# Kernel tuning notes

Hardware: AMD Instinct MI355X
Metric: run time of the kernel (lower is better)

The kernel has to match this reference:

```python
import jax, jax.numpy as jnp
import numpy as np

N_NODES = 50000


def gcn_conv(x, W, b, src, dst, n_nodes):
    # PyG GCNConv: h = D^{-1/2}(A+I)D^{-1/2} X W + b, with self-loops added.
    h = x @ W                                   # [N, H]
    loops = jnp.arange(n_nodes, dtype=src.dtype)
    s = jnp.concatenate([src, loops])           # [E+N]
    d = jnp.concatenate([dst, loops])
    deg = jax.ops.segment_sum(jnp.ones_like(d, dtype=h.dtype), d, num_segments=n_nodes)
    dinv = jnp.where(deg > 0, jax.lax.rsqrt(deg), 0.0)
    norm = dinv[s] * dinv[d]                    # [E+N]
    msg = h[s] * norm[:, None]                  # gather + scale
    agg = jax.ops.segment_sum(msg, d, num_segments=n_nodes)  # scatter-add
    return agg + b


def setup_inputs() -> dict:
    key = jax.random.key(0)
    ks = jax.random.split(key, 8)
    N, E, D, H, ED = N_NODES, 800000, 64, 64, 16
    sc = lambda f_in: 1.0 / np.sqrt(f_in)
    return {
        "x": jax.random.normal(ks[0], (N, D), dtype=jnp.float32),
        "src": jax.random.randint(ks[1], (E,), 0, N),
        "dst": jax.random.randint(ks[2], (E,), 0, N),
        "edge_attr": jax.random.normal(ks[3], (E, ED), dtype=jnp.float32),
        "W1": jax.random.normal(ks[4], (D, H), dtype=jnp.float32) * sc(D),
        "b1": jnp.zeros((H,), dtype=jnp.float32),
        "Wm1": jax.random.normal(ks[5], (2 * H + ED, H), dtype=jnp.float32) * sc(2 * H + ED),
        "bm1": jnp.zeros((H,), dtype=jnp.float32),
        "Wm2": jax.random.normal(ks[6], (H, 1), dtype=jnp.float32) * sc(H),
        "bm2": jnp.zeros((1,), dtype=jnp.float32),
    }


def reference(x, src, dst, edge_attr, W1, b1, Wm1, bm1, Wm2, bm2):
    h = jax.nn.relu(gcn_conv(x, W1, b1, src, dst, N_NODES))  # [N, H]
    edge_repr = jnp.concatenate([h[src], h[dst], edge_attr], axis=1)  # [E, 2H+ED]
    hidden = jax.nn.relu(edge_repr @ Wm1 + bm1)
    scores = jax.nn.sigmoid(hidden @ Wm2 + bm2)
    return scores.squeeze(-1)
```

## Files before the change

kernel.cpp:

```cpp
#include <hip/hip_runtime.h>
#include <math.h>


typedef __attribute__((ext_vector_type(8))) short bf16x8;
typedef __attribute__((ext_vector_type(4))) float f32x4;

#define MAXDEG 64
#define BSHIFT 7
#define BMASK 127
#define NBUCK 391
#define CAP 2560
#define CHUNK 2048
#define BINB 391
#define GEMB 782
#define BPB 40

__device__ __forceinline__ unsigned short f2b(float f) {
    unsigned u = __float_as_uint(f);
    unsigned r = (u + 0x7FFFu + ((u >> 16) & 1u)) >> 16;
    return (unsigned short)r;
}

__global__ void __launch_bounds__(256) bin_gemm_pack(
        const int* __restrict__ dst, const int* __restrict__ src,
        unsigned int* __restrict__ region, int* __restrict__ gcur, int E,
        const float* __restrict__ x, const float* __restrict__ W1,
        unsigned short* __restrict__ gbf,
        const float* __restrict__ Wm1, unsigned short* __restrict__ Bp, int N) {
    __shared__ __align__(16) char smem[8192];
    const int bid = blockIdx.x, tid = threadIdx.x;

    if (bid < BINB) {
        int* lc = (int*)smem;
        int* gb = lc + NBUCK;
        for (int i = tid; i < NBUCK; i += 256) lc[i] = 0;
        __syncthreads();
        int base = bid * CHUNK + tid * 8;
        unsigned key[8], val[8];
#pragma unroll
        for (int k = 0; k < 8; ++k) {
            int e = base + k;
            key[k] = 0xFFFFFFFFu;
            if (e < E) {
                int d = dst[e], s = src[e];
                int b = d >> BSHIFT;
                int r = atomicAdd(&lc[b], 1);
                key[k] = (unsigned)b | ((unsigned)r << 9);
                val[k] = ((unsigned)(d & BMASK) << 16) | (unsigned)s;
            }
        }
        __syncthreads();
        for (int i = tid; i < NBUCK; i += 256) {
            int t = lc[i];
            gb[i] = t ? atomicAdd(&gcur[i], t) : 0;
        }
        __syncthreads();
#pragma unroll
        for (int k = 0; k < 8; ++k) {
            if (key[k] != 0xFFFFFFFFu) {
                int b = (int)(key[k] & 511u), r = (int)(key[k] >> 9);
                int idx = gb[b] + r;
                if (idx < CAP) region[(size_t)b * CAP + idx] = val[k];
            }
        }
    } else if (bid < BINB + GEMB) {
        unsigned short* sB = (unsigned short*)smem;
        for (int i = tid; i < 4096; i += 256) {
            int j = i & 7, ln = (i >> 3) & 63, t = (i >> 9) & 3, s = i >> 11;
            int k = s * 32 + (ln >> 4) * 8 + j, col = t * 16 + (ln & 15);
            sB[i] = f2b(W1[k * 64 + col]);
        }
        __syncthreads();
        int wid = (bid - BINB) * 4 + (tid >> 6);
        int NWT = N / 16;
        if (wid < NWT) {
            int lane = tid & 63, m = lane & 15, quad = lane >> 4;
            int r0 = wid * 16;
            f32x4 acc[4];
#pragma unroll
            for (int t = 0; t < 4; ++t) acc[t] = (f32x4){0.f, 0.f, 0.f, 0.f};
            const bf16x8* bp = (const bf16x8*)sB;
#pragma unroll
            for (int s = 0; s < 2; ++s) {
                const float4* xp = (const float4*)(x + (size_t)(r0 + m) * 64 + s * 32 + quad * 8);
                float4 v0 = xp[0], v1 = xp[1];
                bf16x8 a;
                a[0] = (short)f2b(v0.x); a[1] = (short)f2b(v0.y);
                a[2] = (short)f2b(v0.z); a[3] = (short)f2b(v0.w);
                a[4] = (short)f2b(v1.x); a[5] = (short)f2b(v1.y);
                a[6] = (short)f2b(v1.z); a[7] = (short)f2b(v1.w);
#pragma unroll
                for (int t = 0; t < 4; ++t)
                    acc[t] = __builtin_amdgcn_mfma_f32_16x16x32_bf16(
                        a, bp[(s * 4 + t) * 64 + lane], acc[t], 0, 0, 0);
            }
#pragma unroll
            for (int reg = 0; reg < 4; ++reg) {
                int row = r0 + quad * 4 + reg;
#pragma unroll
                for (int t = 0; t < 4; ++t)
                    gbf[(size_t)row * 64 + t * 16 + m] = f2b(acc[t][reg]);
            }
        }
    } else {
        int idx = (bid - BINB - GEMB) * 256 + tid;
        if (idx < 10240) {
            int j = idx & 7, ln = (idx >> 3) & 63, t = (idx >> 9) & 3, s = idx >> 11;
            int k = s * 32 + (ln >> 4) * 8 + j, col = t * 16 + (ln & 15);
            float v = (k < 144) ? Wm1[k * 64 + col] : 0.0f;
            Bp[idx] = f2b(v);
        }
    }
}

__global__ void __launch_bounds__(256) build_csr(
        const unsigned int* __restrict__ region, const int* __restrict__ gcur,
        int* __restrict__ cnt, unsigned short* __restrict__ csr_pad, int N) {
    __shared__ unsigned short lcsr[128 * MAXDEG];
    __shared__ int lcnt[128];
    int b = blockIdx.x, tid = threadIdx.x;
    if (tid < 128) lcnt[tid] = 0;
    __syncthreads();
    int ecnt = gcur[b]; if (ecnt > CAP) ecnt = CAP;
    const unsigned int* reg = region + (size_t)b * CAP;
    for (int i = tid; i < ecnt; i += 256) {
        unsigned v = reg[i];
        int dloc = (int)(v >> 16), s = (int)(v & 0xFFFFu);
        int r = atomicAdd(&lcnt[dloc], 1);
        if (r < MAXDEG) lcsr[dloc * MAXDEG + r] = (unsigned short)s;
    }
    __syncthreads();
    int n0 = b << BSHIFT;
    int nb = N - n0; if (nb > 128) nb = 128;
    if (tid < nb) cnt[n0 + tid] = lcnt[tid];
    int4* gout = (int4*)(csr_pad + (size_t)n0 * MAXDEG);
    const int4* lin = (const int4*)lcsr;
    int tot = nb * 8;
    for (int i = tid; i < tot; i += 256) gout[i] = lin[i];
}

__global__ void __launch_bounds__(256) gather_finalize(
        const unsigned short* __restrict__ gbf, const unsigned short* __restrict__ csr_pad,
        const int* __restrict__ cnt, const float* __restrict__ b1,
        unsigned short* __restrict__ hbf, int N) {
    int wid = blockIdx.x * 4 + (threadIdx.x >> 6);
    if (wid >= N) return;
    int lane = threadIdx.x & 63;
    int n8 = lane >> 3, c8 = lane & 7;
    int deg = cnt[wid];
    if (deg > MAXDEG) deg = MAXDEG;
    size_t base = (size_t)wid << 6;
    const int4* gb4 = (const int4*)gbf;
    float a[8];
#pragma unroll
    for (int k = 0; k < 8; ++k) a[k] = 0.f;

    for (int j0 = 0; j0 < deg; j0 += 64) {
        int nidx = j0 + lane;
        int sidx = (nidx < deg) ? (int)csr_pad[base + nidx] : 0;
        int c = deg - j0; if (c > 64) c = 64;
        for (int step = 0; step * 8 < c; ++step) {
            int nn = step * 8 + n8;
            int srow = __shfl(sidx, nn, 64);
            int4 u = make_int4(0, 0, 0, 0);
            float ds = 0.f;
            if (nn < c) {
                u = gb4[(size_t)srow * 8 + c8];
                ds = rsqrtf((float)cnt[srow] + 1.0f);
            }
            a[0] += ds * __uint_as_float((unsigned)u.x << 16);
            a[1] += ds * __uint_as_float((unsigned)u.x & 0xffff0000u);
            a[2] += ds * __uint_as_float((unsigned)u.y << 16);
            a[3] += ds * __uint_as_float((unsigned)u.y & 0xffff0000u);
            a[4] += ds * __uint_as_float((unsigned)u.z << 16);
            a[5] += ds * __uint_as_float((unsigned)u.z & 0xffff0000u);
            a[6] += ds * __uint_as_float((unsigned)u.w << 16);
            a[7] += ds * __uint_as_float((unsigned)u.w & 0xffff0000u);
        }
    }
#pragma unroll
    for (int mask = 8; mask < 64; mask <<= 1) {
#pragma unroll
        for (int k = 0; k < 8; ++k) a[k] += __shfl_xor(a[k], mask, 64);
    }
    float dd = rsqrtf((float)deg + 1.0f);
    {
        int4 u = gb4[(size_t)wid * 8 + c8];
        a[0] += dd * __uint_as_float((unsigned)u.x << 16);
        a[1] += dd * __uint_as_float((unsigned)u.x & 0xffff0000u);
        a[2] += dd * __uint_as_float((unsigned)u.y << 16);
        a[3] += dd * __uint_as_float((unsigned)u.y & 0xffff0000u);
        a[4] += dd * __uint_as_float((unsigned)u.z << 16);
        a[5] += dd * __uint_as_float((unsigned)u.z & 0xffff0000u);
        a[6] += dd * __uint_as_float((unsigned)u.w << 16);
        a[7] += dd * __uint_as_float((unsigned)u.w & 0xffff0000u);
    }
    if (n8 == 0) {
        const float4* bv = (const float4*)(b1 + c8 * 8);
        float4 b0 = bv[0], b14 = bv[1];
        float h0 = dd * a[0] + b0.x,  h1 = dd * a[1] + b0.y;
        float h2 = dd * a[2] + b0.z,  h3 = dd * a[3] + b0.w;
        float h4 = dd * a[4] + b14.x, h5 = dd * a[5] + b14.y;
        float h6 = dd * a[6] + b14.z, h7 = dd * a[7] + b14.w;
        h0 = h0 > 0.f ? h0 : 0.f; h1 = h1 > 0.f ? h1 : 0.f;
        h2 = h2 > 0.f ? h2 : 0.f; h3 = h3 > 0.f ? h3 : 0.f;
        h4 = h4 > 0.f ? h4 : 0.f; h5 = h5 > 0.f ? h5 : 0.f;
        h6 = h6 > 0.f ? h6 : 0.f; h7 = h7 > 0.f ? h7 : 0.f;
        int4 w;
        w.x = (int)((unsigned)f2b(h0) | ((unsigned)f2b(h1) << 16));
        w.y = (int)((unsigned)f2b(h2) | ((unsigned)f2b(h3) << 16));
        w.z = (int)((unsigned)f2b(h4) | ((unsigned)f2b(h5) << 16));
        w.w = (int)((unsigned)f2b(h6) | ((unsigned)f2b(h7) << 16));
        ((int4*)hbf)[(size_t)wid * 8 + c8] = w;
    }
}

__global__ void __launch_bounds__(256, 8) edge_mlp_mfma(
        const unsigned short* __restrict__ hbf, const float* __restrict__ ea,
        const int* __restrict__ src, const int* __restrict__ dst,
        const unsigned short* __restrict__ Bp,
        const float* __restrict__ bm1, const float* __restrict__ Wm2,
        const float* __restrict__ bm2, float* __restrict__ out, int E) {
    __shared__ unsigned short sB[10240];
    {
        const int4* gB = (const int4*)Bp;
        int4* lB = (int4*)sB;
#pragma unroll
        for (int i = 0; i < 5; ++i)
            lB[threadIdx.x + i * 256] = gB[threadIdx.x + i * 256];
    }
    __syncthreads();
    int lane = threadIdx.x & 63;
    int wave = threadIdx.x >> 6;
    int m = lane & 15, quad = lane >> 4;
    int e0 = (blockIdx.x * 4 + wave) * 16;
    if (e0 >= E) return;
    int e = e0 + m;
    int ec = e < E ? e : E - 1;
    int si = src[ec], di = dst[ec];
    bf16x8 af[5];
    af[0] = *(const bf16x8*)(hbf + (size_t)si * 64 + quad * 8);
    af[1] = *(const bf16x8*)(hbf + (size_t)si * 64 + 32 + quad * 8);
    af[2] = *(const bf16x8*)(hbf + (size_t)di * 64 + quad * 8);
    af[3] = *(const bf16x8*)(hbf + (size_t)di * 64 + 32 + quad * 8);
    if (quad < 2) {
        const float4* ep = (const float4*)(ea + (size_t)ec * 16 + quad * 8);
        float4 v0 = ep[0], v1 = ep[1];
        af[4][0] = (short)f2b(v0.x); af[4][1] = (short)f2b(v0.y);
        af[4][2] = (short)f2b(v0.z); af[4][3] = (short)f2b(v0.w);
        af[4][4] = (short)f2b(v1.x); af[4][5] = (short)f2b(v1.y);
        af[4][6] = (short)f2b(v1.z); af[4][7] = (short)f2b(v1.w);
    } else {
#pragma unroll
        for (int j = 0; j < 8; ++j) af[4][j] = 0;
    }
    __builtin_amdgcn_sched_barrier(0);
    f32x4 acc[4];
#pragma unroll
    for (int t = 0; t < 4; ++t) acc[t] = (f32x4){0.f, 0.f, 0.f, 0.f};
    const bf16x8* bp = (const bf16x8*)sB;
#pragma unroll
    for (int s = 0; s < 5; ++s) {
#pragma unroll
        for (int t = 0; t < 4; ++t)
            acc[t] = __builtin_amdgcn_mfma_f32_16x16x32_bf16(
                af[s], bp[(s * 4 + t) * 64 + lane], acc[t], 0, 0, 0);
    }
    float w2[4], bb[4];
#pragma unroll
    for (int t = 0; t < 4; ++t) {
        int col = t * 16 + m;
        bb[t] = bm1[col];
        w2[t] = Wm2[col];
    }
    float pr[4];
#pragma unroll
    for (int r = 0; r < 4; ++r) {
        float sum = 0.0f;
#pragma unroll
        for (int t = 0; t < 4; ++t) {
            float hv = acc[t][r] + bb[t];
            sum += (hv > 0.0f ? hv : 0.0f) * w2[t];
        }
        pr[r] = sum;
    }
#pragma unroll
    for (int off = 1; off < 16; off <<= 1) {
#pragma unroll
        for (int r = 0; r < 4; ++r) pr[r] += __shfl_xor(pr[r], off, 64);
    }
    float b2 = bm2[0];
    if (m < 4) {
        int eo = e0 + quad * 4 + m;
        if (eo < E) out[eo] = 1.0f / (1.0f + __expf(-(pr[m] + b2)));
    }
}

extern "C" void kernel_launch(void* const* d_in, const int* in_sizes, int n_in,
                              void* d_out, int out_size, void* d_ws, size_t ws_size,
                              hipStream_t stream) {
    const float* x   = (const float*)d_in[0];
    const int*   src = (const int*)d_in[1];
    const int*   dst = (const int*)d_in[2];
    const float* ea  = (const float*)d_in[3];
    const float* W1  = (const float*)d_in[4];
    const float* b1  = (const float*)d_in[5];
    const float* Wm1 = (const float*)d_in[6];
    const float* bm1 = (const float*)d_in[7];
    const float* Wm2 = (const float*)d_in[8];
    const float* bm2 = (const float*)d_in[9];
    float* out = (float*)d_out;

    int N = in_sizes[0] / 64;
    int E = in_sizes[1];

    char* p = (char*)d_ws;
    unsigned short* gbf     = (unsigned short*)p; p += (size_t)N * 64 * 2;
    unsigned short* hbf     = (unsigned short*)p; p += (size_t)N * 64 * 2;
    unsigned short* csr_pad = (unsigned short*)p; p += (size_t)N * MAXDEG * 2;
    int*            cnt     = (int*)p;            p += (size_t)N * 4;
    int*            gcur    = (int*)p;            p += (size_t)((NBUCK * 4 + 15) / 16) * 16;
    unsigned short* Bp      = (unsigned short*)p; p += 10240 * 2;
    unsigned int*   region  = (unsigned int*)hbf;

    hipMemsetAsync(gcur, 0, NBUCK * sizeof(int), stream);
    bin_gemm_pack<<<BINB + GEMB + BPB, 256, 0, stream>>>(
        dst, src, region, gcur, E, x, W1, gbf, Wm1, Bp, N);
    build_csr<<<NBUCK, 256, 0, stream>>>(region, gcur, cnt, csr_pad, N);
    gather_finalize<<<(N + 3) / 4, 256, 0, stream>>>(gbf, csr_pad, cnt, b1, hbf, N);
    edge_mlp_mfma<<<(E + 63) / 64, 256, 0, stream>>>(hbf, ea, src, dst, Bp,
                                                     bm1, Wm2, bm2, out, E);
}
```

Before: 194.6 us.

## Coalesce edge binning via shared-memory bucket sort and hoist degree lookups

The binning blocks now each take 4096 edges, read dst and src with int4 vector loads, and run a prefix scan in shared memory to sort edges by bucket locally. They then write to the global region in bucket-contiguous order, so global stores are more coalesced than the previous scattered per-thread writes. In the gather kernel, each lane now computes the source-degree rsqrt once and broadcasts it with a shuffle, replacing a repeated per-step load of cnt. In exchange the binning block uses more shared memory and does more syncs, and there are half as many binning blocks. The int4 loads also assume E is a multiple of 4.

```diff
diff --git a/kernel.cpp b/kernel.cpp
--- a/kernel.cpp
+++ b/kernel.cpp
@@ -10,8 +10,8 @@
 #define BMASK 127
 #define NBUCK 391
 #define CAP 2560
-#define CHUNK 2048
-#define BINB 391
+#define CHUNK 4096
+#define BINB 196
 #define GEMB 782
 #define BPB 40
 
@@ -27,41 +27,79 @@
         const float* __restrict__ x, const float* __restrict__ W1,
         unsigned short* __restrict__ gbf,
         const float* __restrict__ Wm1, unsigned short* __restrict__ Bp, int N) {
-    __shared__ __align__(16) char smem[8192];
+    __shared__ __align__(16) char smem[32768];
     const int bid = blockIdx.x, tid = threadIdx.x;
 
     if (bid < BINB) {
         int* lc = (int*)smem;
-        int* gb = lc + NBUCK;
-        for (int i = tid; i < NBUCK; i += 256) lc[i] = 0;
-        __syncthreads();
-        int base = bid * CHUNK + tid * 8;
-        unsigned key[8], val[8];
-#pragma unroll
-        for (int k = 0; k < 8; ++k) {
-            int e = base + k;
-            key[k] = 0xFFFFFFFFu;
-            if (e < E) {
-                int d = dst[e], s = src[e];
-                int b = d >> BSHIFT;
-                int r = atomicAdd(&lc[b], 1);
-                key[k] = (unsigned)b | ((unsigned)r << 9);
-                val[k] = ((unsigned)(d & BMASK) << 16) | (unsigned)s;
-            }
-        }
-        __syncthreads();
+        int* s0 = lc + 512;
+        int* s1 = s0 + 512;
+        int* gb = s1 + 512;
+        unsigned* lval = (unsigned*)(gb + 512);
+        unsigned short* lbuk = (unsigned short*)(lval + 4096);
+
+        for (int i = tid; i < 512; i += 256) lc[i] = 0;
+        __syncthreads();
+
+        unsigned kb[16], kv[16];
+#pragma unroll
+        for (int j = 0; j < 4; ++j) {
+            int i4 = bid * 1024 + j * 256 + tid;
+            bool ok = (i4 * 4 < E);
+            int4 d4 = make_int4(0, 0, 0, 0), s4 = make_int4(0, 0, 0, 0);
+            if (ok) { d4 = ((const int4*)dst)[i4]; s4 = ((const int4*)src)[i4]; }
+            int dd[4] = {d4.x, d4.y, d4.z, d4.w};
+            int ss[4] = {s4.x, s4.y, s4.z, s4.w};
+#pragma unroll
+            for (int k = 0; k < 4; ++k) {
+                int idx = j * 4 + k;
+                kb[idx] = 0xFFFFFFFFu;
+                if (ok) {
+                    int b = dd[k] >> BSHIFT;
+                    int r = atomicAdd(&lc[b], 1);
+                    kb[idx] = ((unsigned)b << 12) | (unsigned)r;
+                    kv[idx] = ((unsigned)(dd[k] & BMASK) << 16) | (unsigned)ss[k];
+                }
+            }
+        }
+        __syncthreads();
+
+        for (int i = tid; i < 512; i += 256) s0[i] = lc[i];
+        __syncthreads();
+        int* pin = s0; int* pout = s1;
+        for (int off = 1; off < 512; off <<= 1) {
+            for (int i = tid; i < 512; i += 256) {
+                int v = pin[i];
+                if (i >= off) v += pin[i - off];
+                pout[i] = v;
+            }
+            __syncthreads();
+            int* t = pin; pin = pout; pout = t;
+        }
+        int* lb = pout;
+        for (int i = tid; i < 512; i += 256) lb[i] = pin[i] - lc[i];
         for (int i = tid; i < NBUCK; i += 256) {
-            int t = lc[i];
-            gb[i] = t ? atomicAdd(&gcur[i], t) : 0;
-        }
-        __syncthreads();
-#pragma unroll
-        for (int k = 0; k < 8; ++k) {
-            if (key[k] != 0xFFFFFFFFu) {
-                int b = (int)(key[k] & 511u), r = (int)(key[k] >> 9);
-                int idx = gb[b] + r;
-                if (idx < CAP) region[(size_t)b * CAP + idx] = val[k];
-            }
+            int c = lc[i];
+            gb[i] = c ? atomicAdd(&gcur[i], c) : 0;
+        }
+        __syncthreads();
+
+#pragma unroll
+        for (int idx = 0; idx < 16; ++idx) {
+            if (kb[idx] != 0xFFFFFFFFu) {
+                int b = (int)(kb[idx] >> 12), r = (int)(kb[idx] & 4095u);
+                int pos = lb[b] + r;
+                lval[pos] = kv[idx];
+                lbuk[pos] = (unsigned short)b;
+            }
+        }
+        __syncthreads();
+
+        int ne = E - bid * CHUNK; if (ne > CHUNK) ne = CHUNK;
+        for (int i = tid; i < ne; i += 256) {
+            int b = lbuk[i];
+            int idx = gb[b] + (i - lb[b]);
+            if (idx < CAP) region[(size_t)b * CAP + idx] = lval[i];
         }
     } else if (bid < BINB + GEMB) {
         unsigned short* sB = (unsigned short*)smem;
@@ -157,17 +195,18 @@
 
     for (int j0 = 0; j0 < deg; j0 += 64) {
         int nidx = j0 + lane;
-        int sidx = (nidx < deg) ? (int)csr_pad[base + nidx] : 0;
+        int sidx = 0; float dsv = 0.f;
+        if (nidx < deg) {
+            sidx = (int)csr_pad[base + nidx];
+            dsv = rsqrtf((float)cnt[sidx] + 1.0f);
+        }
         int c = deg - j0; if (c > 64) c = 64;
         for (int step = 0; step * 8 < c; ++step) {
             int nn = step * 8 + n8;
             int srow = __shfl(sidx, nn, 64);
+            float ds = __shfl(dsv, nn, 64);
             int4 u = make_int4(0, 0, 0, 0);
-            float ds = 0.f;
-            if (nn < c) {
-                u = gb4[(size_t)srow * 8 + c8];
-                ds = rsqrtf((float)cnt[srow] + 1.0f);
-            }
+            if (nn < c) u = gb4[(size_t)srow * 8 + c8];
             a[0] += ds * __uint_as_float((unsigned)u.x << 16);
             a[1] += ds * __uint_as_float((unsigned)u.x & 0xffff0000u);
             a[2] += ds * __uint_as_float((unsigned)u.y << 16);
```

New measurement: 190.7 us. -2.0%, faster.
